# Kernel tuning notes

Hardware: AMD Instinct MI355X
Metric: run time of the kernel (lower is better)

Reference implementation:

```python
import jax, jax.numpy as jnp
import numpy as np

N4, N3, N2, N1, K = 32768, 65536, 131072, 262144, 16
G = 512


def _w(key, fan_in, fan_out):
    return jax.random.normal(key, (fan_in, fan_out), dtype=jnp.float32) / np.sqrt(fan_in)


def setup_inputs() -> dict:
    key = jax.random.key(0)
    ks = jax.random.split(key, 24)

    def edges(k, n_coarse, n_fine):
        # each fine (output) point gathers from K random coarse (input) points
        src = jax.random.randint(k, (n_fine * K,), 0, n_coarse, dtype=jnp.int32)
        dst = jnp.repeat(jnp.arange(n_fine, dtype=jnp.int32), K)
        return src, dst

    src3, dst3 = edges(ks[0], N4, N3)
    src2, dst2 = edges(ks[1], N3, N2)
    src1, dst1 = edges(ks[2], N2, N1)

    def gidx(k, n):
        return jnp.sort(jax.random.randint(k, (n,), 0, G, dtype=jnp.int32))

    inp = {
        'z_mask': jax.random.normal(ks[3], (N4, 64), dtype=jnp.float32),
        'pos4': jax.random.normal(ks[4], (N4, 3), dtype=jnp.float32),
        'pos3': jax.random.normal(ks[5], (N3, 3), dtype=jnp.float32),
        'pos2': jax.random.normal(ks[6], (N2, 3), dtype=jnp.float32),
        'pos1': jax.random.normal(ks[7], (N1, 3), dtype=jnp.float32),
        'g4': gidx(ks[8], N4), 'g3': gidx(ks[9], N3),
        'g2': gidx(ks[10], N2), 'g1': gidx(ks[11], N1),
        # PointConv MLP params: Linear(c_in+3 -> c_mid), CELU, Linear(c_mid -> c_out), max-aggregate
        'w1a': _w(ks[12], 64 + 3, 64), 'b1a': jnp.zeros((64,), jnp.float32),
        'w1b': _w(ks[13], 64, 32), 'b1b': jnp.zeros((32,), jnp.float32),
        'w2a': _w(ks[14], 32 + 3, 16), 'b2a': jnp.zeros((16,), jnp.float32),
        'w2b': _w(ks[15], 16, 16), 'b2b': jnp.zeros((16,), jnp.float32),
        'w3a': _w(ks[16], 16 + 3, 8), 'b3a': jnp.zeros((8,), jnp.float32),
        'w3b': _w(ks[17], 8, 8), 'b3b': jnp.zeros((8,), jnp.float32),
        'wlin': _w(ks[18], 8, 1), 'blin': jnp.zeros((1,), jnp.float32),
        'src3': src3, 'dst3': dst3,
        'src2': src2, 'dst2': dst2,
        'src1': src1, 'dst1': dst1,
    }
    return inp


def point_conv(x_in, pos_in, pos_out, src, dst, w_a, b_a, w_b, b_b, n_out):
    # gather: per-edge neighbor features + relative positions
    rel = pos_in[src] - pos_out[dst]                      # [E, 3]
    feat = jnp.concatenate([x_in[src], rel], axis=-1)     # [E, c_in+3]
    h = jax.nn.celu(feat @ w_a + b_a)                     # [E, c_mid]
    m = h @ w_b + b_b                                     # [E, c_out]
    # scatter: max-aggregate edge messages onto output points
    return jax.ops.segment_max(m, dst, num_segments=n_out)


def reference(z_mask, pos4, pos3, pos2, pos1, g4, g3, g2, g1,
              w1a, b1a, w1b, b1b, w2a, b2a, w2b, b2b, w3a, b3a, w3b, b3b,
              wlin, blin, src3, dst3, src2, dst2, src1, dst1):
    out = jax.nn.celu(point_conv(z_mask, pos4, pos3, src3, dst3, w1a, b1a, w1b, b1b, N3))
    out = jax.nn.celu(point_conv(out, pos3, pos2, src2, dst2, w2a, b2a, w2b, b2b, N2))
    out = jax.nn.celu(point_conv(out, pos2, pos1, src1, dst1, w3a, b3a, w3b, b3b, N1))
    logits = out @ wlin + blin                            # [N1, 1]
    return jax.nn.log_sigmoid(logits)
```

## Files before the change

### kernel.cpp

```cpp
#include <hip/hip_runtime.h>
#include <hip/hip_fp16.h>
#include <math.h>

#define N4C 32768
#define N3C 65536
#define N2C 131072
#define N1C 262144

typedef _Float16 f16x8 __attribute__((ext_vector_type(8)));
typedef float f32x4 __attribute__((ext_vector_type(4)));
typedef float f32x16 __attribute__((ext_vector_type(16)));

__device__ __forceinline__ f32x4 mfma16(f16x8 a, f16x8 b, f32x4 c) {
  return __builtin_amdgcn_mfma_f32_16x16x32_f16(a, b, c, 0, 0, 0);
}
__device__ __forceinline__ f32x16 mfma32(f16x8 a, f16x8 b, f32x16 c) {
  return __builtin_amdgcn_mfma_f32_32x32x16_f16(a, b, c, 0, 0, 0);
}

__device__ __forceinline__ float celuf(float x) {
  return fmaxf(x, 0.f) + (__expf(fminf(x, 0.f)) - 1.f);
}

__device__ __forceinline__ float logsigf(float x) {
  float e = __expf(-fabsf(x));
  return fminf(x, 0.f) - __logf(1.f + e);
}

__device__ __forceinline__ _Float16 exp16(_Float16 x) {
  __half h; __builtin_memcpy(&h, &x, 2);
  h = hexp(h);
  _Float16 r; __builtin_memcpy(&r, &h, 2);
  return r;
}

__device__ __forceinline__ f16x8 celu8(f16x8 x) {
  f16x8 z = {};
  f16x8 mx = __builtin_elementwise_max(x, z);
  f16x8 mn = __builtin_elementwise_min(x, z);
#pragma unroll
  for (int i = 0; i < 8; ++i) mn[i] = exp16(mn[i]);
  return mx + (mn - (_Float16)1.0f);
}

__global__ __launch_bounds__(256) void y4_kernel(
    const float* __restrict__ z, const float* __restrict__ pos4,
    const float* __restrict__ w1a, const float* __restrict__ b1a,
    _Float16* __restrict__ y4) {
  const int lane = threadIdx.x & 63, wid = threadIdx.x >> 6;
  const int col = lane & 15, quad = lane >> 4;
  const int base = (blockIdx.x * 4 + wid) * 16;

  f16x8 Ba[2][4];
#pragma unroll
  for (int c = 0; c < 2; ++c)
#pragma unroll
    for (int t = 0; t < 4; ++t)
#pragma unroll
      for (int j = 0; j < 8; ++j)
        Ba[c][t][j] = (_Float16)w1a[(c * 32 + quad * 8 + j) * 64 + t * 16 + col];

  float wr[3][4];
#pragma unroll
  for (int c = 0; c < 3; ++c)
#pragma unroll
    for (int t = 0; t < 4; ++t)
      wr[c][t] = w1a[(64 + c) * 64 + t * 16 + col];

  float px[4], py[4], pz[4];
#pragma unroll
  for (int r = 0; r < 4; ++r) {
    const int row = base + quad * 4 + r;
    px[r] = pos4[row * 3 + 0];
    py[r] = pos4[row * 3 + 1];
    pz[r] = pos4[row * 3 + 2];
  }

  const float* zr = z + (size_t)(base + col) * 64;
  f16x8 A0, A1;
  {
    float4 f0 = *(const float4*)(zr + quad * 8);
    float4 f1 = *(const float4*)(zr + quad * 8 + 4);
    float4 f2 = *(const float4*)(zr + 32 + quad * 8);
    float4 f3 = *(const float4*)(zr + 32 + quad * 8 + 4);
    A0[0] = (_Float16)f0.x; A0[1] = (_Float16)f0.y; A0[2] = (_Float16)f0.z; A0[3] = (_Float16)f0.w;
    A0[4] = (_Float16)f1.x; A0[5] = (_Float16)f1.y; A0[6] = (_Float16)f1.z; A0[7] = (_Float16)f1.w;
    A1[0] = (_Float16)f2.x; A1[1] = (_Float16)f2.y; A1[2] = (_Float16)f2.z; A1[3] = (_Float16)f2.w;
    A1[4] = (_Float16)f3.x; A1[5] = (_Float16)f3.y; A1[6] = (_Float16)f3.z; A1[7] = (_Float16)f3.w;
  }
#pragma unroll
  for (int t = 0; t < 4; ++t) {
    f32x4 acc = {0.f, 0.f, 0.f, 0.f};
    acc = mfma16(A0, Ba[0][t], acc);
    acc = mfma16(A1, Ba[1][t], acc);
    const float bt = b1a[t * 16 + col];
#pragma unroll
    for (int r = 0; r < 4; ++r) {
      const float posterm =
          px[r] * wr[0][t] + py[r] * wr[1][t] + pz[r] * wr[2][t];
      y4[(size_t)(base + quad * 4 + r) * 64 + t * 16 + col] =
          (_Float16)(acc[r] + bt + posterm);
    }
  }
}

__global__ __launch_bounds__(256) void y3_kernel(
    const _Float16* __restrict__ x3f, const float* __restrict__ pos3,
    const float* __restrict__ w2a, const float* __restrict__ b2a,
    _Float16* __restrict__ y3) {
  const int lane = threadIdx.x & 63, wid = threadIdx.x >> 6;
  const int col = lane & 15, quad = lane >> 4;
  const int base = (blockIdx.x * 4 + wid) * 16;

  f16x8 B;
#pragma unroll
  for (int j = 0; j < 8; ++j) B[j] = (_Float16)w2a[(quad * 8 + j) * 16 + col];

  float wr[3];
#pragma unroll
  for (int c = 0; c < 3; ++c) wr[c] = w2a[(32 + c) * 16 + col];

  float px[4], py[4], pz[4];
#pragma unroll
  for (int r = 0; r < 4; ++r) {
    const int row = base + quad * 4 + r;
    px[r] = pos3[row * 3 + 0];
    py[r] = pos3[row * 3 + 1];
    pz[r] = pos3[row * 3 + 2];
  }

  f16x8 A = *(const f16x8*)(x3f + (size_t)(base + col) * 32 + quad * 8);
  f32x4 d = {0.f, 0.f, 0.f, 0.f};
  d = mfma16(A, B, d);
  const float bt = b2a[col];
#pragma unroll
  for (int r = 0; r < 4; ++r) {
    const float posterm = px[r] * wr[0] + py[r] * wr[1] + pz[r] * wr[2];
    y3[(size_t)(base + quad * 4 + r) * 16 + col] =
        (_Float16)(d[r] + bt + posterm);
  }
}

__global__ __launch_bounds__(256) void y2_kernel(
    const _Float16* __restrict__ x2f, const float* __restrict__ pos2,
    const float* __restrict__ w3a, const float* __restrict__ b3a,
    _Float16* __restrict__ y2) {
  const int lane = threadIdx.x & 63, wid = threadIdx.x >> 6;
  const int col = lane & 15, quad = lane >> 4;
  const int base = (blockIdx.x * 4 + wid) * 16;

  f16x8 B;
#pragma unroll
  for (int j = 0; j < 8; ++j) {
    int k = quad * 8 + j;
    B[j] = (k < 16 && col < 8) ? (_Float16)w3a[k * 8 + col] : (_Float16)0.f;
  }
  f16x8 A = *(const f16x8*)(x2f + (size_t)(base + col) * 16 + (quad & 1) * 8);
  f32x4 d = {0.f, 0.f, 0.f, 0.f};
  d = mfma16(A, B, d);
  if (col < 8) {
    float wr[3];
#pragma unroll
    for (int c = 0; c < 3; ++c) wr[c] = w3a[(16 + c) * 8 + col];
    const float bt = b3a[col];
#pragma unroll
    for (int r = 0; r < 4; ++r) {
      const int row = base + quad * 4 + r;
      const float posterm = pos2[row * 3 + 0] * wr[0] +
                            pos2[row * 3 + 1] * wr[1] +
                            pos2[row * 3 + 2] * wr[2];
      y2[(size_t)row * 8 + col] = (_Float16)(d[r] + bt + posterm);
    }
  }
}

__global__ __launch_bounds__(256) void l3_kernel(
    const _Float16* __restrict__ y4, const float* __restrict__ pos3,
    const int* __restrict__ src3, const float* __restrict__ w1a,
    const float* __restrict__ w1b, const float* __restrict__ b1b,
    _Float16* __restrict__ x3f) {
  const int lane = threadIdx.x & 63, wid = threadIdx.x >> 6;
  const int col = lane & 15, quad = lane >> 4;

  f16x8 Bb[2][2];
#pragma unroll
  for (int c = 0; c < 2; ++c)
#pragma unroll
    for (int t = 0; t < 2; ++t)
#pragma unroll
      for (int j = 0; j < 8; ++j)
        Bb[c][t][j] = (_Float16)w1b[(c * 32 + quad * 8 + j) * 32 + t * 16 + col];
  f16x8 W0[3], W1[3];
#pragma unroll
  for (int c = 0; c < 3; ++c)
#pragma unroll
    for (int j = 0; j < 8; ++j) {
      W0[c][j] = (_Float16)w1a[(64 + c) * 64 + quad * 8 + j];
      W1[c][j] = (_Float16)w1a[(64 + c) * 64 + 32 + quad * 8 + j];
    }
  const float biasB0 = b1b[col], biasB1 = b1b[16 + col];

  const int gwave = blockIdx.x * 4 + wid;
  const int nw = gridDim.x * 4;

  for (int p = gwave; p < N3C; p += nw) {
    const int s = src3[p * 16 + col];
    const int up = __builtin_amdgcn_readfirstlane(p);
    const _Float16 q0 = (_Float16)pos3[up * 3 + 0];
    const _Float16 q1 = (_Float16)pos3[up * 3 + 1];
    const _Float16 q2 = (_Float16)pos3[up * 3 + 2];

    f16x8 A0 = *(const f16x8*)(y4 + (size_t)s * 64 + quad * 8);
    f16x8 A1 = *(const f16x8*)(y4 + (size_t)s * 64 + 32 + quad * 8);

    const f16x8 v0 = W0[0] * q0 + W0[1] * q1 + W0[2] * q2;
    const f16x8 v1 = W1[0] * q0 + W1[1] * q1 + W1[2] * q2;

    A0 = celu8(A0 - v0);
    A1 = celu8(A1 - v1);

    f32x4 e[2];
#pragma unroll
    for (int t = 0; t < 2; ++t) {
      f32x4 acc = {0.f, 0.f, 0.f, 0.f};
      acc = mfma16(A0, Bb[0][t], acc);
      acc = mfma16(A1, Bb[1][t], acc);
      e[t] = acc;
    }
    float m0 = fmaxf(fmaxf(e[0][0], e[0][1]), fmaxf(e[0][2], e[0][3]));
    float m1 = fmaxf(fmaxf(e[1][0], e[1][1]), fmaxf(e[1][2], e[1][3]));
    m0 = fmaxf(m0, __shfl_xor(m0, 16, 64));
    m0 = fmaxf(m0, __shfl_xor(m0, 32, 64));
    m1 = fmaxf(m1, __shfl_xor(m1, 16, 64));
    m1 = fmaxf(m1, __shfl_xor(m1, 32, 64));
    if (lane < 16) {
      _Float16* row = x3f + (size_t)p * 32;
      row[col]      = (_Float16)celuf(m0 + biasB0);
      row[16 + col] = (_Float16)celuf(m1 + biasB1);
    }
  }
}

__global__ __launch_bounds__(256) void l2_kernel(
    const _Float16* __restrict__ y3, const float* __restrict__ pos2,
    const int* __restrict__ src2, const float* __restrict__ w2a,
    const float* __restrict__ w2b, const float* __restrict__ b2b,
    _Float16* __restrict__ x2f) {
  const int lane = threadIdx.x & 63, wid = threadIdx.x >> 6;
  const int n = lane & 31;
  const int e = lane & 15;
  const int h = (lane >> 4) & 1;
  const int kh = lane >> 5;

  f16x8 Bb;
#pragma unroll
  for (int j = 0; j < 8; ++j)
    Bb[j] = (n < 16) ? (_Float16)w2b[(kh * 8 + j) * 16 + n] : (_Float16)0.f;
  f16x8 W[3];
#pragma unroll
  for (int c = 0; c < 3; ++c)
#pragma unroll
    for (int j = 0; j < 8; ++j)
      W[c][j] = (_Float16)w2a[(32 + c) * 16 + kh * 8 + j];
  const float biasB = b2b[n & 15];

  const int gwave = blockIdx.x * 4 + wid;
  const int nw = gridDim.x * 4;

  for (int pr = gwave; pr < N2C / 2; pr += nw) {
    const int p = 2 * pr + h;
    const int s = src2[p * 16 + e];

    const _Float16 q0 = (_Float16)pos2[p * 3 + 0];
    const _Float16 q1 = (_Float16)pos2[p * 3 + 1];
    const _Float16 q2 = (_Float16)pos2[p * 3 + 2];

    f16x8 A = *(const f16x8*)(y3 + (size_t)s * 16 + kh * 8);
    const f16x8 v = W[0] * q0 + W[1] * q1 + W[2] * q2;
    A = celu8(A - v);

    f32x16 acc = {};
    acc = mfma32(A, Bb, acc);

    float mA = acc[0], mB = acc[8];
#pragma unroll
    for (int r = 1; r < 8; ++r) {
      mA = fmaxf(mA, acc[r]);
      mB = fmaxf(mB, acc[8 + r]);
    }
    mA = fmaxf(mA, __shfl_xor(mA, 32, 64));
    mB = fmaxf(mB, __shfl_xor(mB, 32, 64));

    if (n < 16) {
      const float m = kh ? mB : mA;
      x2f[(size_t)(2 * pr + kh) * 16 + n] = (_Float16)celuf(m + biasB);
    }
  }
}

__global__ __launch_bounds__(256) void l1_kernel(
    const _Float16* __restrict__ y2, const float* __restrict__ pos1,
    const int* __restrict__ src1, const float* __restrict__ w3a,
    const float* __restrict__ w3b, const float* __restrict__ b3b,
    const float* __restrict__ wlin, const float* __restrict__ blin,
    float* __restrict__ out) {
  const int lane = threadIdx.x & 63, wid = threadIdx.x >> 6;
  const int m = lane & 31;
  const int e = lane & 15;
  const int h = (lane >> 4) & 1;
  const int kh = lane >> 5;
  const int g = 2 * kh + h;

  f16x8 Bb;
  const int n = m;
#pragma unroll
  for (int j = 0; j < 8; ++j)
    Bb[j] = (n < 16 && (n >> 3) == kh) ? (_Float16)w3b[j * 8 + (n & 7)]
                                       : (_Float16)0.f;
  f16x8 W[3];
#pragma unroll
  for (int c = 0; c < 3; ++c)
#pragma unroll
    for (int j = 0; j < 8; ++j)
      W[c][j] = (_Float16)w3a[(16 + c) * 8 + j];
  const float biasB = (n < 16) ? b3b[n & 7] : 0.f;
  const float wl = (n < 16) ? wlin[n & 7] : 0.f;
  const float bl = blin[0];

  const int gwave = blockIdx.x * 4 + wid;
  const int nw = gridDim.x * 4;

  for (int q = gwave; q < N1C / 4; q += nw) {
    const int pb = q * 4;
    const int p = pb + g;
    const int s = src1[p * 16 + e];

    const _Float16 q0 = (_Float16)pos1[p * 3 + 0];
    const _Float16 q1 = (_Float16)pos1[p * 3 + 1];
    const _Float16 q2 = (_Float16)pos1[p * 3 + 2];

    f16x8 A = *(const f16x8*)(y2 + (size_t)s * 8);
    const f16x8 v = W[0] * q0 + W[1] * q1 + W[2] * q2;
    A = celu8(A - v);

    f32x16 acc = {};
    acc = mfma32(A, Bb, acc);

    float mA = acc[0], mB = acc[8];
#pragma unroll
    for (int r = 1; r < 8; ++r) {
      mA = fmaxf(mA, acc[r]);
      mB = fmaxf(mB, acc[8 + r]);
    }
    mA = fmaxf(mA, __shfl_xor(mA, 32, 64));
    mB = fmaxf(mB, __shfl_xor(mB, 32, 64));
    float tA = celuf(mA + biasB) * wl;
    float tB = celuf(mB + biasB) * wl;
    tA += __shfl_xor(tA, 1, 64);
    tA += __shfl_xor(tA, 2, 64);
    tA += __shfl_xor(tA, 4, 64);
    tB += __shfl_xor(tB, 1, 64);
    tB += __shfl_xor(tB, 2, 64);
    tB += __shfl_xor(tB, 4, 64);
    if (lane == 0) {
      float2 o; o.x = logsigf(tA + bl); o.y = logsigf(tB + bl);
      *(float2*)(out + pb) = o;
    } else if (lane == 8) {
      float2 o; o.x = logsigf(tA + bl); o.y = logsigf(tB + bl);
      *(float2*)(out + pb + 2) = o;
    }
  }
}

extern "C" void kernel_launch(void* const* d_in, const int* in_sizes, int n_in,
                              void* d_out, int out_size, void* d_ws, size_t ws_size,
                              hipStream_t stream) {
  const float* z_mask = (const float*)d_in[0];
  const float* pos4 = (const float*)d_in[1];
  const float* pos3 = (const float*)d_in[2];
  const float* pos2 = (const float*)d_in[3];
  const float* pos1 = (const float*)d_in[4];
  const float* w1a = (const float*)d_in[9];
  const float* b1a = (const float*)d_in[10];
  const float* w1b = (const float*)d_in[11];
  const float* b1b = (const float*)d_in[12];
  const float* w2a = (const float*)d_in[13];
  const float* b2a = (const float*)d_in[14];
  const float* w2b = (const float*)d_in[15];
  const float* b2b = (const float*)d_in[16];
  const float* w3a = (const float*)d_in[17];
  const float* b3a = (const float*)d_in[18];
  const float* w3b = (const float*)d_in[19];
  const float* b3b = (const float*)d_in[20];
  const float* wlin = (const float*)d_in[21];
  const float* blin = (const float*)d_in[22];
  const int* src3 = (const int*)d_in[23];
  const int* src2 = (const int*)d_in[25];
  const int* src1 = (const int*)d_in[27];

  char* w = (char*)d_ws;
  _Float16* y4  = (_Float16*)(w);
  _Float16* x3f = (_Float16*)(w + (4u << 20));
  _Float16* y3  = (_Float16*)(w + (8u << 20));
  _Float16* x2f = (_Float16*)(w + (10u << 20));
  _Float16* y2  = (_Float16*)(w + (14u << 20));
  float* out = (float*)d_out;

  y4_kernel<<<512, 256, 0, stream>>>(z_mask, pos4, w1a, b1a, y4);
  l3_kernel<<<2048, 256, 0, stream>>>(y4, pos3, src3, w1a, w1b, b1b, x3f);
  y3_kernel<<<1024, 256, 0, stream>>>(x3f, pos3, w2a, b2a, y3);
  l2_kernel<<<8192, 256, 0, stream>>>(y3, pos2, src2, w2a, w2b, b2b, x2f);
  y2_kernel<<<2048, 256, 0, stream>>>(x2f, pos2, w3a, b3a, y2);
  l1_kernel<<<8192, 256, 0, stream>>>(y2, pos1, src1, w3a, w3b, b3b,
                                      wlin, blin, out);
}
```

Baseline: 251.9 us.

## Unroll gather loops by two, fold CELU -1 into bias, use exp2

Each gather-MLP-max kernel (l3, l2, l1) now handles two output points per loop iteration, issuing both gathers before either compute so more memory latency overlaps. The constant -1 in the CELU is folded into the second-layer bias by subtracting the column sums of the second weight matrix. The f16 exp becomes exp2 with a pre-scale, and the max reductions use 3-input max. Grid sizes for l2 and l1 drop from 8192 to 2048 blocks, so each wave loops more; the exp2 change adds a small rounding difference.

```diff
diff --git a/kernel.cpp b/kernel.cpp
--- a/kernel.cpp
+++ b/kernel.cpp
@@ -27,20 +27,24 @@
   return fminf(x, 0.f) - __logf(1.f + e);
 }
 
-__device__ __forceinline__ _Float16 exp16(_Float16 x) {
+__device__ __forceinline__ float max3f(float a, float b, float c) {
+  return fmaxf(fmaxf(a, b), c);
+}
+
+__device__ __forceinline__ _Float16 exp2_16(_Float16 x) {
   __half h; __builtin_memcpy(&h, &x, 2);
-  h = hexp(h);
+  h = hexp2(h);
   _Float16 r; __builtin_memcpy(&r, &h, 2);
   return r;
 }
 
-__device__ __forceinline__ f16x8 celu8(f16x8 x) {
+__device__ __forceinline__ f16x8 celu8p1(f16x8 x) {
   f16x8 z = {};
   f16x8 mx = __builtin_elementwise_max(x, z);
-  f16x8 mn = __builtin_elementwise_min(x, z);
-#pragma unroll
-  for (int i = 0; i < 8; ++i) mn[i] = exp16(mn[i]);
-  return mx + (mn - (_Float16)1.0f);
+  f16x8 mn = __builtin_elementwise_min(x, z) * (_Float16)1.44269504f;
+#pragma unroll
+  for (int i = 0; i < 8; ++i) mn[i] = exp2_16(mn[i]);
+  return mx + mn;
 }
 
 __global__ __launch_bounds__(256) void y4_kernel(
@@ -174,6 +178,33 @@
   }
 }
 
+__device__ __forceinline__ void l3_compute(
+    int p, f16x8 A0, f16x8 A1, _Float16 q0, _Float16 q1, _Float16 q2,
+    const f16x8 W0[3], const f16x8 W1[3], const f16x8 Bb[2][2],
+    float biasB0, float biasB1, int lane, int col,
+    _Float16* __restrict__ x3f) {
+  A0 = celu8p1(A0 - (W0[0] * q0 + W0[1] * q1 + W0[2] * q2));
+  A1 = celu8p1(A1 - (W1[0] * q0 + W1[1] * q1 + W1[2] * q2));
+
+  f32x4 e0 = {0.f, 0.f, 0.f, 0.f}, e1 = {0.f, 0.f, 0.f, 0.f};
+  e0 = mfma16(A0, Bb[0][0], e0);
+  e0 = mfma16(A1, Bb[1][0], e0);
+  e1 = mfma16(A0, Bb[0][1], e1);
+  e1 = mfma16(A1, Bb[1][1], e1);
+
+  float m0 = fmaxf(max3f(e0[0], e0[1], e0[2]), e0[3]);
+  float m1 = fmaxf(max3f(e1[0], e1[1], e1[2]), e1[3]);
+  m0 = fmaxf(m0, __shfl_xor(m0, 16, 64));
+  m0 = fmaxf(m0, __shfl_xor(m0, 32, 64));
+  m1 = fmaxf(m1, __shfl_xor(m1, 16, 64));
+  m1 = fmaxf(m1, __shfl_xor(m1, 32, 64));
+  if (lane < 16) {
+    _Float16* row = x3f + (size_t)p * 32;
+    row[col]      = (_Float16)celuf(m0 + biasB0);
+    row[16 + col] = (_Float16)celuf(m1 + biasB1);
+  }
+}
+
 __global__ __launch_bounds__(256) void l3_kernel(
     const _Float16* __restrict__ y4, const float* __restrict__ pos3,
     const int* __restrict__ src3, const float* __restrict__ w1a,
@@ -198,46 +229,62 @@
       W0[c][j] = (_Float16)w1a[(64 + c) * 64 + quad * 8 + j];
       W1[c][j] = (_Float16)w1a[(64 + c) * 64 + 32 + quad * 8 + j];
     }
-  const float biasB0 = b1b[col], biasB1 = b1b[16 + col];
+  float s0 = 0.f, s1 = 0.f;
+#pragma unroll 4
+  for (int k = 0; k < 64; ++k) {
+    s0 += w1b[k * 32 + col];
+    s1 += w1b[k * 32 + 16 + col];
+  }
+  const float biasB0 = b1b[col] - s0, biasB1 = b1b[16 + col] - s1;
 
   const int gwave = blockIdx.x * 4 + wid;
-  const int nw = gridDim.x * 4;
-
-  for (int p = gwave; p < N3C; p += nw) {
-    const int s = src3[p * 16 + col];
-    const int up = __builtin_amdgcn_readfirstlane(p);
-    const _Float16 q0 = (_Float16)pos3[up * 3 + 0];
-    const _Float16 q1 = (_Float16)pos3[up * 3 + 1];
-    const _Float16 q2 = (_Float16)pos3[up * 3 + 2];
-
-    f16x8 A0 = *(const f16x8*)(y4 + (size_t)s * 64 + quad * 8);
-    f16x8 A1 = *(const f16x8*)(y4 + (size_t)s * 64 + 32 + quad * 8);
-
-    const f16x8 v0 = W0[0] * q0 + W0[1] * q1 + W0[2] * q2;
-    const f16x8 v1 = W1[0] * q0 + W1[1] * q1 + W1[2] * q2;
-
-    A0 = celu8(A0 - v0);
-    A1 = celu8(A1 - v1);
-
-    f32x4 e[2];
-#pragma unroll
-    for (int t = 0; t < 2; ++t) {
-      f32x4 acc = {0.f, 0.f, 0.f, 0.f};
-      acc = mfma16(A0, Bb[0][t], acc);
-      acc = mfma16(A1, Bb[1][t], acc);
-      e[t] = acc;
-    }
-    float m0 = fmaxf(fmaxf(e[0][0], e[0][1]), fmaxf(e[0][2], e[0][3]));
-    float m1 = fmaxf(fmaxf(e[1][0], e[1][1]), fmaxf(e[1][2], e[1][3]));
-    m0 = fmaxf(m0, __shfl_xor(m0, 16, 64));
-    m0 = fmaxf(m0, __shfl_xor(m0, 32, 64));
-    m1 = fmaxf(m1, __shfl_xor(m1, 16, 64));
-    m1 = fmaxf(m1, __shfl_xor(m1, 32, 64));
-    if (lane < 16) {
-      _Float16* row = x3f + (size_t)p * 32;
-      row[col]      = (_Float16)celuf(m0 + biasB0);
-      row[16 + col] = (_Float16)celuf(m1 + biasB1);
-    }
+  const int nw = gridDim.x << 2;
+
+#pragma unroll 1
+  for (int p = gwave; p < N3C; p += 2 * nw) {
+    const int p2 = p + nw;
+    const int upa = __builtin_amdgcn_readfirstlane(p);
+    const int upb = __builtin_amdgcn_readfirstlane(p2);
+    const int sa = src3[p * 16 + col];
+    const int sb = src3[p2 * 16 + col];
+
+    f16x8 A0a = *(const f16x8*)(y4 + (size_t)sa * 64 + quad * 8);
+    f16x8 A1a = *(const f16x8*)(y4 + (size_t)sa * 64 + 32 + quad * 8);
+    f16x8 A0b = *(const f16x8*)(y4 + (size_t)sb * 64 + quad * 8);
+    f16x8 A1b = *(const f16x8*)(y4 + (size_t)sb * 64 + 32 + quad * 8);
+
+    const _Float16 qa0 = (_Float16)pos3[upa * 3 + 0];
+    const _Float16 qa1 = (_Float16)pos3[upa * 3 + 1];
+    const _Float16 qa2 = (_Float16)pos3[upa * 3 + 2];
+    const _Float16 qb0 = (_Float16)pos3[upb * 3 + 0];
+    const _Float16 qb1 = (_Float16)pos3[upb * 3 + 1];
+    const _Float16 qb2 = (_Float16)pos3[upb * 3 + 2];
+
+    l3_compute(p,  A0a, A1a, qa0, qa1, qa2, W0, W1, Bb, biasB0, biasB1,
+               lane, col, x3f);
+    l3_compute(p2, A0b, A1b, qb0, qb1, qb2, W0, W1, Bb, biasB0, biasB1,
+               lane, col, x3f);
+  }
+}
+
+__device__ __forceinline__ void l2_compute(
+    int pr, f16x8 A_in, _Float16 q0, _Float16 q1, _Float16 q2,
+    const f16x8 W[3], f16x8 Bb, float biasB, int kh, int n,
+    _Float16* __restrict__ x2f) {
+  f16x8 A = celu8p1(A_in - (W[0] * q0 + W[1] * q1 + W[2] * q2));
+  f32x16 acc = {};
+  acc = mfma32(A, Bb, acc);
+
+  float mA = fmaxf(max3f(max3f(acc[0], acc[1], acc[2]),
+                         max3f(acc[3], acc[4], acc[5]), acc[6]), acc[7]);
+  float mB = fmaxf(max3f(max3f(acc[8], acc[9], acc[10]),
+                         max3f(acc[11], acc[12], acc[13]), acc[14]), acc[15]);
+  mA = fmaxf(mA, __shfl_xor(mA, 32, 64));
+  mB = fmaxf(mB, __shfl_xor(mB, 32, 64));
+
+  if (n < 16) {
+    const float m = kh ? mB : mA;
+    x2f[(size_t)(2 * pr + kh) * 16 + n] = (_Float16)celuf(m + biasB);
   }
 }
 
@@ -262,39 +309,65 @@
 #pragma unroll
     for (int j = 0; j < 8; ++j)
       W[c][j] = (_Float16)w2a[(32 + c) * 16 + kh * 8 + j];
-  const float biasB = b2b[n & 15];
+  float ws = 0.f;
+#pragma unroll
+  for (int k = 0; k < 16; ++k) ws += w2b[k * 16 + (n & 15)];
+  const float biasB = b2b[n & 15] - ws;
 
   const int gwave = blockIdx.x * 4 + wid;
-  const int nw = gridDim.x * 4;
-
-  for (int pr = gwave; pr < N2C / 2; pr += nw) {
-    const int p = 2 * pr + h;
-    const int s = src2[p * 16 + e];
-
-    const _Float16 q0 = (_Float16)pos2[p * 3 + 0];
-    const _Float16 q1 = (_Float16)pos2[p * 3 + 1];
-    const _Float16 q2 = (_Float16)pos2[p * 3 + 2];
-
-    f16x8 A = *(const f16x8*)(y3 + (size_t)s * 16 + kh * 8);
-    const f16x8 v = W[0] * q0 + W[1] * q1 + W[2] * q2;
-    A = celu8(A - v);
-
-    f32x16 acc = {};
-    acc = mfma32(A, Bb, acc);
-
-    float mA = acc[0], mB = acc[8];
-#pragma unroll
-    for (int r = 1; r < 8; ++r) {
-      mA = fmaxf(mA, acc[r]);
-      mB = fmaxf(mB, acc[8 + r]);
-    }
-    mA = fmaxf(mA, __shfl_xor(mA, 32, 64));
-    mB = fmaxf(mB, __shfl_xor(mB, 32, 64));
-
-    if (n < 16) {
-      const float m = kh ? mB : mA;
-      x2f[(size_t)(2 * pr + kh) * 16 + n] = (_Float16)celuf(m + biasB);
-    }
+  const int nw = gridDim.x << 2;
+
+#pragma unroll 1
+  for (int pr = gwave; pr < N2C / 2; pr += 2 * nw) {
+    const int pr2 = pr + nw;
+    const int pa = 2 * pr + h, pb = 2 * pr2 + h;
+    const int sa = src2[pa * 16 + e];
+    const int sb = src2[pb * 16 + e];
+
+    f16x8 Aa = *(const f16x8*)(y3 + (size_t)sa * 16 + kh * 8);
+    f16x8 Ab = *(const f16x8*)(y3 + (size_t)sb * 16 + kh * 8);
+
+    const _Float16 qa0 = (_Float16)pos2[pa * 3 + 0];
+    const _Float16 qa1 = (_Float16)pos2[pa * 3 + 1];
+    const _Float16 qa2 = (_Float16)pos2[pa * 3 + 2];
+    const _Float16 qb0 = (_Float16)pos2[pb * 3 + 0];
+    const _Float16 qb1 = (_Float16)pos2[pb * 3 + 1];
+    const _Float16 qb2 = (_Float16)pos2[pb * 3 + 2];
+
+    l2_compute(pr,  Aa, qa0, qa1, qa2, W, Bb, biasB, kh, n, x2f);
+    l2_compute(pr2, Ab, qb0, qb1, qb2, W, Bb, biasB, kh, n, x2f);
+  }
+}
+
+__device__ __forceinline__ void l1_compute(
+    int pb, f16x8 A_in, _Float16 q0, _Float16 q1, _Float16 q2,
+    const f16x8 W[3], f16x8 Bb, float biasB, float wl, float bl, int lane,
+    float* __restrict__ out) {
+  f16x8 A = celu8p1(A_in - (W[0] * q0 + W[1] * q1 + W[2] * q2));
+  f32x16 acc = {};
+  acc = mfma32(A, Bb, acc);
+
+  float mA = fmaxf(max3f(max3f(acc[0], acc[1], acc[2]),
+                         max3f(acc[3], acc[4], acc[5]), acc[6]), acc[7]);
+  float mB = fmaxf(max3f(max3f(acc[8], acc[9], acc[10]),
+                         max3f(acc[11], acc[12], acc[13]), acc[14]), acc[15]);
+  mA = fmaxf(mA, __shfl_xor(mA, 32, 64));
+  mB = fmaxf(mB, __shfl_xor(mB, 32, 64));
+
+  float tA = celuf(mA + biasB) * wl;
+  float tB = celuf(mB + biasB) * wl;
+  tA += __shfl_xor(tA, 1, 64);
+  tA += __shfl_xor(tA, 2, 64);
+  tA += __shfl_xor(tA, 4, 64);
+  tB += __shfl_xor(tB, 1, 64);
+  tB += __shfl_xor(tB, 2, 64);
+  tB += __shfl_xor(tB, 4, 64);
+  if (lane == 0) {
+    float2 o; o.x = logsigf(tA + bl); o.y = logsigf(tB + bl);
+    *(float2*)(out + pb) = o;
+  } else if (lane == 8) {
+    float2 o; o.x = logsigf(tA + bl); o.y = logsigf(tB + bl);
+    *(float2*)(out + pb + 2) = o;
   }
 }
 
@@ -323,52 +396,36 @@
 #pragma unroll
     for (int j = 0; j < 8; ++j)
       W[c][j] = (_Float16)w3a[(16 + c) * 8 + j];
-  const float biasB = (n < 16) ? b3b[n & 7] : 0.f;
+  float ws = 0.f;
+#pragma unroll
+  for (int j = 0; j < 8; ++j) ws += w3b[j * 8 + (n & 7)];
+  const float biasB = (n < 16) ? b3b[n & 7] - ws : 0.f;
   const float wl = (n < 16) ? wlin[n & 7] : 0.f;
   const float bl = blin[0];
 
   const int gwave = blockIdx.x * 4 + wid;
-  const int nw = gridDim.x * 4;
-
-  for (int q = gwave; q < N1C / 4; q += nw) {
-    const int pb = q * 4;
-    const int p = pb + g;
-    const int s = src1[p * 16 + e];
-
-    const _Float16 q0 = (_Float16)pos1[p * 3 + 0];
-    const _Float16 q1 = (_Float16)pos1[p * 3 + 1];
-    const _Float16 q2 = (_Float16)pos1[p * 3 + 2];
-
-    f16x8 A = *(const f16x8*)(y2 + (size_t)s * 8);
-    const f16x8 v = W[0] * q0 + W[1] * q1 + W[2] * q2;
-    A = celu8(A - v);
-
-    f32x16 acc = {};
-    acc = mfma32(A, Bb, acc);
-
-    float mA = acc[0], mB = acc[8];
-#pragma unroll
-    for (int r = 1; r < 8; ++r) {
-      mA = fmaxf(mA, acc[r]);
-      mB = fmaxf(mB, acc[8 + r]);
-    }
-    mA = fmaxf(mA, __shfl_xor(mA, 32, 64));
-    mB = fmaxf(mB, __shfl_xor(mB, 32, 64));
-    float tA = celuf(mA + biasB) * wl;
-    float tB = celuf(mB + biasB) * wl;
-    tA += __shfl_xor(tA, 1, 64);
-    tA += __shfl_xor(tA, 2, 64);
-    tA += __shfl_xor(tA, 4, 64);
-    tB += __shfl_xor(tB, 1, 64);
-    tB += __shfl_xor(tB, 2, 64);
-    tB += __shfl_xor(tB, 4, 64);
-    if (lane == 0) {
-      float2 o; o.x = logsigf(tA + bl); o.y = logsigf(tB + bl);
-      *(float2*)(out + pb) = o;
-    } else if (lane == 8) {
-      float2 o; o.x = logsigf(tA + bl); o.y = logsigf(tB + bl);
-      *(float2*)(out + pb + 2) = o;
-    }
+  const int nw = gridDim.x << 2;
+
+#pragma unroll 1
+  for (int q = gwave; q < N1C / 4; q += 2 * nw) {
+    const int q2 = q + nw;
+    const int pba = q * 4, pbb = q2 * 4;
+    const int pa = pba + g, pb = pbb + g;
+    const int sa = src1[pa * 16 + e];
+    const int sb = src1[pb * 16 + e];
+
+    f16x8 Aa = *(const f16x8*)(y2 + (size_t)sa * 8);
+    f16x8 Ab = *(const f16x8*)(y2 + (size_t)sb * 8);
+
+    const _Float16 qa0 = (_Float16)(pos1[pa * 3 + 0]);
+    const _Float16 qa1 = (_Float16)(pos1[pa * 3 + 1]);
+    const _Float16 qa2 = (_Float16)(pos1[pa * 3 + 2]);
+    const _Float16 qb0 = (_Float16)(pos1[pb * 3 + 0]);
+    const _Float16 qb1 = (_Float16)(pos1[pb * 3 + 1]);
+    const _Float16 qb2 = (_Float16)(pos1[pb * 3 + 2]);
+
+    l1_compute(pba, Aa, qa0, qa1, qa2, W, Bb, biasB, wl, bl, lane, out);
+    l1_compute(pbb, Ab, qb0, qb1, qb2, W, Bb, biasB, wl, bl, lane, out);
   }
 }
 
@@ -409,8 +466,8 @@
   y4_kernel<<<512, 256, 0, stream>>>(z_mask, pos4, w1a, b1a, y4);
   l3_kernel<<<2048, 256, 0, stream>>>(y4, pos3, src3, w1a, w1b, b1b, x3f);
   y3_kernel<<<1024, 256, 0, stream>>>(x3f, pos3, w2a, b2a, y3);
-  l2_kernel<<<8192, 256, 0, stream>>>(y3, pos2, src2, w2a, w2b, b2b, x2f);
+  l2_kernel<<<2048, 256, 0, stream>>>(y3, pos2, src2, w2a, w2b, b2b, x2f);
   y2_kernel<<<2048, 256, 0, stream>>>(x2f, pos2, w3a, b3a, y2);
-  l1_kernel<<<8192, 256, 0, stream>>>(y2, pos1, src1, w3a, w3b, b3b,
+  l1_kernel<<<2048, 256, 0, stream>>>(y2, pos1, src1, w3a, w3b, b3b,
                                       wlin, blin, out);
 }
```

After: 242.5 us. -3.7%, faster.
